# Optimization experiments

Measured on AMD Instinct MI355X. Metric: run time of the kernel, lower is better.

Reference implementation:

```python
import jax, jax.numpy as jnp
import numpy as np

B, C, H, W = 16, 3, 224, 224
P = 16
DIM = 256
NL = 8
DS = 16          # d_state (mamba default)
DCONV = 4
NCLS = 1000
DI = 2 * DIM     # expand * dim
DTR = -(-DIM // 16)  # dt_rank = ceil(dim/16)
NPATCH = (H // P) * (W // P)
SEQ = NPATCH + 1


def _ln(x, g, b, eps=1e-5):
    mu = x.mean(-1, keepdims=True)
    var = ((x - mu) ** 2).mean(-1, keepdims=True)
    return (x - mu) * jax.lax.rsqrt(var + eps) * g + b


def setup_inputs() -> dict:
    key = jax.random.key(0)
    ks = jax.random.split(key, 12)
    pd = C * P * P
    s = 0.02
    return dict(
        img=jax.random.normal(ks[0], (B, C, H, W), jnp.float32),
        pe_ln1_g=jnp.ones((pd,), jnp.float32), pe_ln1_b=jnp.zeros((pd,), jnp.float32),
        pe_w=jax.random.normal(ks[1], (pd, DIM), jnp.float32) * s,
        pe_b=jnp.zeros((DIM,), jnp.float32),
        pe_ln2_g=jnp.ones((DIM,), jnp.float32), pe_ln2_b=jnp.zeros((DIM,), jnp.float32),
        pos_emb=jax.random.normal(ks[2], (1, SEQ, DIM), jnp.float32) * s,
        cls_tok=jax.random.normal(ks[3], (1, 1, DIM), jnp.float32) * s,
        ln_w=jnp.ones((NL, DIM), jnp.float32), ln_b=jnp.zeros((NL, DIM), jnp.float32),
        in_w=jax.random.normal(ks[4], (NL, DIM, 2 * DI), jnp.float32) * s,
        conv_w=jax.random.normal(ks[5], (NL, DI, DCONV), jnp.float32) * s,
        conv_b=jnp.zeros((NL, DI), jnp.float32),
        xproj_w=jax.random.normal(ks[6], (NL, DI, DTR + 2 * DS), jnp.float32) * s,
        dtproj_w=jax.random.normal(ks[7], (NL, DTR, DI), jnp.float32) * s,
        dtproj_b=jax.random.uniform(ks[8], (NL, DI), jnp.float32, -4.0, -2.0),
        A_log=jnp.log(jnp.broadcast_to(jnp.arange(1, DS + 1, dtype=jnp.float32), (NL, DI, DS))) + jnp.zeros((NL, DI, DS), jnp.float32),
        Dp=jnp.ones((NL, DI), jnp.float32),
        out_w=jax.random.normal(ks[9], (NL, DI, DIM), jnp.float32) * s,
        normf_w=jnp.ones((DIM,), jnp.float32), normf_b=jnp.zeros((DIM,), jnp.float32),
        head_w=jax.random.normal(ks[10], (DIM, NCLS), jnp.float32) * s,
        head_b=jnp.zeros((NCLS,), jnp.float32),
    )


def _mamba(x, in_w, conv_w, conv_b, xproj_w, dtproj_w, dtproj_b, A_log, Dp, out_w):
    b, L, _ = x.shape
    xz = x @ in_w                       # (b, L, 2*DI)
    xm, z = jnp.split(xz, 2, axis=-1)
    # causal depthwise conv1d (torch pads both sides then slices -> left-pad d_conv-1)
    xc = jnp.pad(xm.transpose(0, 2, 1), ((0, 0), (0, 0), (DCONV - 1, 0)))
    xc = jax.lax.conv_general_dilated(
        xc, conv_w[:, None, :], (1,), 'VALID',
        dimension_numbers=('NCH', 'OIH', 'NCH'), feature_group_count=DI)
    u = jax.nn.silu(xc + conv_b[None, :, None]).transpose(0, 2, 1)  # (b, L, DI)
    dbc = u @ xproj_w                   # (b, L, DTR+2*DS)
    dt, Bm, Cm = jnp.split(dbc, [DTR, DTR + DS], axis=-1)
    dt = jax.nn.softplus(dt @ dtproj_w + dtproj_b)  # (b, L, DI)
    A = -jnp.exp(A_log)                 # (DI, DS)

    def step(h, inp):
        dt_t, B_t, C_t, u_t = inp       # (b,DI), (b,DS), (b,DS), (b,DI)
        dA = jnp.exp(dt_t[:, :, None] * A)                 # (b, DI, DS)
        h = dA * h + (dt_t * u_t)[:, :, None] * B_t[:, None, :]
        y = jnp.einsum('bdn,bn->bd', h, C_t)
        return h, y

    h0 = jnp.zeros((b, DI, DS), x.dtype)
    xs = (dt.transpose(1, 0, 2), Bm.transpose(1, 0, 2),
          Cm.transpose(1, 0, 2), u.transpose(1, 0, 2))
    _, ys = jax.lax.scan(step, h0, xs)
    y = ys.transpose(1, 0, 2) + u * Dp  # (b, L, DI)
    y = y * jax.nn.silu(z)
    return y @ out_w                    # (b, L, DIM)


def reference(img, pe_ln1_g, pe_ln1_b, pe_w, pe_b, pe_ln2_g, pe_ln2_b, pos_emb,
              cls_tok, ln_w, ln_b, in_w, conv_w, conv_b, xproj_w, dtproj_w,
              dtproj_b, A_log, Dp, out_w, normf_w, normf_b, head_w, head_b):
    b = img.shape[0]
    h, w = H // P, W // P
    # 'b c (h p1) (w p2) -> b (h w) (p1 p2 c)'
    x = img.reshape(b, C, h, P, w, P).transpose(0, 2, 4, 3, 5, 1).reshape(b, h * w, P * P * C)
    x = _ln(x, pe_ln1_g, pe_ln1_b)
    x = x @ pe_w + pe_b
    x = _ln(x, pe_ln2_g, pe_ln2_b)
    x = jnp.concatenate([jnp.broadcast_to(cls_tok, (b, 1, DIM)), x], axis=1)
    x = x + pos_emb[:, :x.shape[1]]
    residual = None
    for i in range(NL):
        residual = x if residual is None else x + residual
        xn = _ln(residual, ln_w[i], ln_b[i])
        x = _mamba(xn, in_w[i], conv_w[i], conv_b[i], xproj_w[i],
                   dtproj_w[i], dtproj_b[i], A_log[i], Dp[i], out_w[i])
    residual = x + residual
    x = _ln(residual, normf_w, normf_b)
    x = x[:, 0]                          # pool == 'cls'
    return x @ head_w + head_b
```

## Files before the change

### kernel.cpp

```cpp
#include <hip/hip_runtime.h>
#include <math.h>

#define NB   16
#define SEQL 197
#define TB   (NB*SEQL)
#define DIMM 256
#define DI   512
#define DS   16
#define NL   8

typedef __bf16 bf16x8 __attribute__((ext_vector_type(8)));
typedef __bf16 bf16x4 __attribute__((ext_vector_type(4)));
typedef float floatx4 __attribute__((ext_vector_type(4)));

__device__ __forceinline__ void block_reduce_2(float& s1, float& s2, float* red, int tid){
  #pragma unroll
  for (int off = 32; off > 0; off >>= 1){
    s1 += __shfl_down(s1, off, 64);
    s2 += __shfl_down(s2, off, 64);
  }
  __syncthreads();
  if ((tid & 63) == 0){ red[(tid>>6)*2] = s1; red[(tid>>6)*2+1] = s2; }
  __syncthreads();
  s1 = red[0] + red[2] + red[4] + red[6];
  s2 = red[1] + red[3] + red[5] + red[7];
}

__global__ __launch_bounds__(256) void transpose_bf16(
    const float* __restrict__ in, __bf16* __restrict__ out, int K, int N)
{
  __shared__ float t[32][33];
  const float* src = in  + (size_t)blockIdx.z*K*N;
  __bf16*      dst = out + (size_t)blockIdx.z*K*N;
  int n0 = blockIdx.x*32, k0 = blockIdx.y*32;
  int tx = threadIdx.x & 31, ty = threadIdx.x >> 5;
  #pragma unroll
  for (int j = 0; j < 4; j++)
    t[ty + j*8][tx] = src[(size_t)(k0 + ty + j*8)*N + n0 + tx];
  __syncthreads();
  #pragma unroll
  for (int j = 0; j < 4; j++)
    dst[(size_t)(n0 + ty + j*8)*K + k0 + tx] = (__bf16)t[tx][ty + j*8];
}

__global__ __launch_bounds__(256) void transpose_bf16_pad(
    const float* __restrict__ in, __bf16* __restrict__ out, int K, int Nin, int Npad)
{
  __shared__ float t[32][33];
  const float* src = in  + (size_t)blockIdx.z*K*Nin;
  __bf16*      dst = out + (size_t)blockIdx.z*Npad*K;
  int n0 = blockIdx.x*32, k0 = blockIdx.y*32;
  int tx = threadIdx.x & 31, ty = threadIdx.x >> 5;
  #pragma unroll
  for (int j = 0; j < 4; j++){
    int n = n0 + tx;
    t[ty + j*8][tx] = (n < Nin) ? src[(size_t)(k0 + ty + j*8)*Nin + n] : 0.f;
  }
  __syncthreads();
  #pragma unroll
  for (int j = 0; j < 4; j++)
    dst[(size_t)(n0 + ty + j*8)*K + k0 + tx] = (__bf16)t[tx][ty + j*8];
}

template<int BM, int BN>
__global__ __launch_bounds__(256) void gemm_bf16(
    const __bf16* __restrict__ A, const __bf16* __restrict__ Wt,
    const float* __restrict__ bias, float* __restrict__ C, int M, int N, int K)
{
  constexpr int BK  = 32;
  constexpr int LDA = BK + 8;
  constexpr int TMW = BM/32;
  constexpr int TNW = BN/32;
  __shared__ __bf16 As[BM][LDA];
  __shared__ __bf16 Bs[BN][LDA];

  int tid  = threadIdx.x;
  int lane = tid & 63, w = tid >> 6;
  int wm = w >> 1, wn = w & 1;
  int l15 = lane & 15, quad = lane >> 4;
  int bm = blockIdx.y * BM, bn = blockIdx.x * BN;

  floatx4 acc[TMW][TNW] = {};

  for (int k0 = 0; k0 < K; k0 += BK){
    #pragma unroll
    for (int i = 0; i < BM/64; i++){
      int c = tid + i*256;
      int row = c >> 2, kc = c & 3;
      int m = bm + row;
      uint4 v = make_uint4(0,0,0,0);
      if (m < M) v = ((const uint4*)(A + (size_t)m*K + k0))[kc];
      *(uint4*)&As[row][kc*8] = v;
    }
    #pragma unroll
    for (int i = 0; i < BN/64; i++){
      int c = tid + i*256;
      int row = c >> 2, kc = c & 3;
      int n = bn + row;
      uint4 v = ((const uint4*)(Wt + (size_t)n*K + k0))[kc];
      *(uint4*)&Bs[row][kc*8] = v;
    }
    __syncthreads();
    bf16x8 af[TMW], bf[TNW];
    #pragma unroll
    for (int mi = 0; mi < TMW; mi++)
      af[mi] = *(const bf16x8*)&As[wm*(BM/2) + mi*16 + l15][quad*8];
    #pragma unroll
    for (int ni = 0; ni < TNW; ni++)
      bf[ni] = *(const bf16x8*)&Bs[wn*(BN/2) + ni*16 + l15][quad*8];
    #pragma unroll
    for (int mi = 0; mi < TMW; mi++)
      #pragma unroll
      for (int ni = 0; ni < TNW; ni++)
        acc[mi][ni] = __builtin_amdgcn_mfma_f32_16x16x32_bf16(af[mi], bf[ni], acc[mi][ni], 0, 0, 0);
    __syncthreads();
  }
  #pragma unroll
  for (int mi = 0; mi < TMW; mi++){
    #pragma unroll
    for (int ni = 0; ni < TNW; ni++){
      int col = bn + wn*(BN/2) + ni*16 + l15;
      float bv = bias ? bias[col] : 0.f;
      #pragma unroll
      for (int r = 0; r < 4; r++){
        int row = bm + wm*(BM/2) + mi*16 + quad*4 + r;
        if (row < M) C[(size_t)row*N + col] = acc[mi][ni][r] + bv;
      }
    }
  }
}

__global__ __launch_bounds__(256) void patch_ln1(
    const float* __restrict__ img, const float* __restrict__ g1, const float* __restrict__ b1,
    __bf16* __restrict__ xp_bf)
{
  __shared__ float red[8];
  int blk = blockIdx.x;
  int b = blk / 196, p = blk % 196;
  int hh = p / 14, ww = p % 14;
  int tid = threadIdx.x;

  float v[3]; float s = 0.f, s2 = 0.f;
  #pragma unroll
  for (int i = 0; i < 3; i++){
    int e  = tid + i*256;
    int c  = e % 3;
    int p2 = (e/3) % 16;
    int p1 = e / 48;
    float val = img[((b*3 + c)*224 + hh*16 + p1)*224 + ww*16 + p2];
    v[i] = val; s += val; s2 += val*val;
  }
  block_reduce_2(s, s2, red, tid);
  float mu = s * (1.f/768.f);
  float var = s2 * (1.f/768.f) - mu*mu;
  float rr = rsqrtf(var + 1e-5f);
  #pragma unroll
  for (int i = 0; i < 3; i++){
    int e = tid + i*256;
    xp_bf[(size_t)blk*768 + e] = (__bf16)((v[i] - mu) * rr * g1[e] + b1[e]);
  }
}

__global__ __launch_bounds__(256) void ln2_pos(
    const float* __restrict__ pemb, const float* __restrict__ g2, const float* __restrict__ b2,
    const float* __restrict__ pos, float* __restrict__ x)
{
  __shared__ float red[8];
  int blk = blockIdx.x;
  int b = blk / 196, p = blk % 196;
  int tid = threadIdx.x;
  float v = pemb[(size_t)blk*256 + tid];
  float s = v, s2 = v*v;
  block_reduce_2(s, s2, red, tid);
  float mu = s * (1.f/256.f);
  float var = s2 * (1.f/256.f) - mu*mu;
  float rr = rsqrtf(var + 1e-5f);
  float o = (v - mu) * rr * g2[tid] + b2[tid] + pos[(1+p)*256 + tid];
  x[((size_t)(b*SEQL + 1 + p))*256 + tid] = o;
}

__global__ __launch_bounds__(256) void cls_pos(
    const float* __restrict__ cls, const float* __restrict__ pos, float* __restrict__ x)
{
  int b = blockIdx.x, tid = threadIdx.x;
  x[(size_t)b*SEQL*256 + tid] = cls[tid] + pos[tid];
}

__global__ __launch_bounds__(256) void add_ln(
    const float* __restrict__ x, float* __restrict__ resid, __bf16* __restrict__ xn_bf,
    const float* __restrict__ g, const float* __restrict__ bta, int first)
{
  int w = threadIdx.x >> 6, l = threadIdx.x & 63;
  int t = blockIdx.x*4 + w;
  size_t base = (size_t)t*256 + l*4;
  float4 xv = *(const float4*)&x[base];
  if (!first){
    float4 rv = *(const float4*)&resid[base];
    xv.x += rv.x; xv.y += rv.y; xv.z += rv.z; xv.w += rv.w;
  }
  *(float4*)&resid[base] = xv;
  float s  = xv.x + xv.y + xv.z + xv.w;
  float s2 = xv.x*xv.x + xv.y*xv.y + xv.z*xv.z + xv.w*xv.w;
  #pragma unroll
  for (int off = 1; off < 64; off <<= 1){
    s  += __shfl_xor(s,  off, 64);
    s2 += __shfl_xor(s2, off, 64);
  }
  float mu = s * (1.f/256.f);
  float var = s2 * (1.f/256.f) - mu*mu;
  float rr = rsqrtf(var + 1e-5f);
  float4 gv = *(const float4*)&g[l*4];
  float4 bv = *(const float4*)&bta[l*4];
  bf16x4 o;
  o[0] = (__bf16)((xv.x - mu)*rr*gv.x + bv.x);
  o[1] = (__bf16)((xv.y - mu)*rr*gv.y + bv.y);
  o[2] = (__bf16)((xv.z - mu)*rr*gv.z + bv.z);
  o[3] = (__bf16)((xv.w - mu)*rr*gv.w + bv.w);
  *(bf16x4*)&xn_bf[base] = o;
}

__global__ __launch_bounds__(256) void conv_silu(
    const float* __restrict__ xz, const float* __restrict__ cw, const float* __restrict__ cb,
    float* __restrict__ u, __bf16* __restrict__ u_bf)
{
  int gid = blockIdx.x*256 + threadIdx.x;
  if (gid >= TB*DI) return;
  int d = gid & 511;
  int t = gid >> 9;
  int l = t % SEQL;
  float acc = cb[d];
  if (l >= 3) acc += xz[(size_t)(t-3)*1024 + d] * cw[d*4+0];
  if (l >= 2) acc += xz[(size_t)(t-2)*1024 + d] * cw[d*4+1];
  if (l >= 1) acc += xz[(size_t)(t-1)*1024 + d] * cw[d*4+2];
  acc += xz[(size_t)t*1024 + d] * cw[d*4+3];
  float sg = 1.f / (1.f + __expf(-acc));
  float val = acc * sg;
  u[(size_t)t*512 + d] = val;
  u_bf[(size_t)t*512 + d] = (__bf16)val;
}

#define SCT 32
#define NCH ((SEQL + SCT - 1)/SCT)
__global__ __launch_bounds__(256) void scan_kernel(
    const float* __restrict__ u, const float* __restrict__ dbc,
    const float* __restrict__ xz, const float* __restrict__ A_log, const float* __restrict__ Dp,
    const float* __restrict__ dtw, const float* __restrict__ dtb,
    __bf16* __restrict__ yg_bf)
{
  __shared__ float s_D [16][36];
  __shared__ float s_B [16][36];
  __shared__ float s_C [16][36];
  __shared__ float s_u [16][36];
  __shared__ float s_z [16][36];
  __shared__ float s_dt[16][36];
  __shared__ float s_yp[SCT][16][20];
  __shared__ float s_dp[16];

  int tid = threadIdx.x;
  int n = tid & 15, dl = tid >> 4;
  int b = blockIdx.x >> 5, dg = blockIdx.x & 31;
  int d0 = dg * 16;
  const size_t base = (size_t)b * SEQL;

  float A = -__expf(A_log[(d0+dl)*DS + n]);
  float h = 0.f;
  if (tid < 16) s_dp[tid] = Dp[d0 + tid];
  float wc[16];
  #pragma unroll
  for (int k = 0; k < 16; k++) wc[k] = dtw[k*512 + d0 + n];
  float dtbv = dtb[d0 + n];

  float r_u[2], r_z[2], r_db[6];
  auto load_regs = [&](int c){
    #pragma unroll
    for (int i = 0; i < 2; i++){
      int v = tid + i*256;
      int tg = c*SCT + (v>>4); if (tg > SEQL-1) tg = SEQL-1;
      size_t t = base + tg;
      r_u[i] = u [t*512 + d0 + (v&15)];
      r_z[i] = xz[t*1024 + 512 + d0 + (v&15)];
    }
    #pragma unroll
    for (int s = 0; s < 3; s++)
      #pragma unroll
      for (int i = 0; i < 2; i++){
        int v = tid + i*256;
        int tg = c*SCT + (v>>4); if (tg > SEQL-1) tg = SEQL-1;
        r_db[s*2+i] = dbc[(base + tg)*64 + s*16 + (v&15)];
      }
  };
  auto write_DBC = [&](){
    #pragma unroll
    for (int i = 0; i < 2; i++){
      int v = tid + i*256;
      s_D[v&15][v>>4] = r_db[0+i];
      s_B[v&15][v>>4] = r_db[2+i];
      s_C[v&15][v>>4] = r_db[4+i];
    }
  };
  auto write_UZ = [&](){
    #pragma unroll
    for (int i = 0; i < 2; i++){
      int v = tid + i*256;
      s_u[v&15][v>>4] = r_u[i];
      s_z[v&15][v>>4] = r_z[i];
    }
  };
  auto compute_dt = [&](){
    #pragma unroll
    for (int i = 0; i < 2; i++){
      int tl = (tid >> 4) + i*16;
      float acc = dtbv;
      #pragma unroll
      for (int k = 0; k < 16; k++) acc += s_D[k][tl] * wc[k];
      s_dt[n][tl] = (acc > 20.f) ? acc : log1pf(__expf(acc));
    }
  };

  load_regs(0);
  write_DBC();
  write_UZ();
  __syncthreads();
  compute_dt();
  __syncthreads();

  for (int c = 0; c < NCH; c++){
    if (c + 1 < NCH) load_regs(c+1);

    float4 dt4, u4, B4, C4;
    #pragma unroll
    for (int tl = 0; tl < SCT; tl++){
      if ((tl & 3) == 0){
        dt4 = *(const float4*)&s_dt[dl][tl];
        u4  = *(const float4*)&s_u [dl][tl];
        B4  = *(const float4*)&s_B [n][tl];
        C4  = *(const float4*)&s_C [n][tl];
      }
      float dtv = ((float*)&dt4)[tl&3];
      float uv  = ((float*)&u4 )[tl&3];
      float Bv  = ((float*)&B4 )[tl&3];
      float Cv  = ((float*)&C4 )[tl&3];
      h = __expf(dtv * A) * h + (dtv * uv) * Bv;
      s_yp[tl][dl][n] = h * Cv;
    }
    __syncthreads();

    if (c + 1 < NCH) write_DBC();

    #pragma unroll
    for (int j = 0; j < 2; j++){
      int p = tid + j*256;
      int tl = p >> 4, dr = p & 15;
      float4 a0 = *(const float4*)&s_yp[tl][dr][0];
      float4 a1 = *(const float4*)&s_yp[tl][dr][4];
      float4 a2 = *(const float4*)&s_yp[tl][dr][8];
      float4 a3 = *(const float4*)&s_yp[tl][dr][12];
      float yv = ((a0.x+a0.y)+(a0.z+a0.w)) + ((a1.x+a1.y)+(a1.z+a1.w))
               + ((a2.x+a2.y)+(a2.z+a2.w)) + ((a3.x+a3.y)+(a3.z+a3.w));
      int tg = c*SCT + tl;
      if (tg < SEQL){
        float uv = s_u[dr][tl];
        float zv = s_z[dr][tl];
        float sg = 1.f / (1.f + __expf(-zv));
        yg_bf[(base + tg)*512 + d0 + dr] = (__bf16)((yv + uv*s_dp[dr]) * zv * sg);
      }
    }
    __syncthreads();

    if (c + 1 < NCH){
      write_UZ();
      compute_dt();
      __syncthreads();
    }
  }
}

__global__ __launch_bounds__(256) void final_ln(
    const float* __restrict__ x, const float* __restrict__ resid,
    const float* __restrict__ g, const float* __restrict__ bta, float* __restrict__ xs_g)
{
  __shared__ float red[8];
  int b = blockIdx.x, tid = threadIdx.x;
  size_t idx = (size_t)b*SEQL*256 + tid;
  float r = x[idx] + resid[idx];
  float s = r, s2 = r*r;
  block_reduce_2(s, s2, red, tid);
  float mu = s * (1.f/256.f);
  float var = s2 * (1.f/256.f) - mu*mu;
  float rr = rsqrtf(var + 1e-5f);
  xs_g[b*256 + tid] = (r - mu) * rr * g[tid] + bta[tid];
}

__global__ __launch_bounds__(256) void head_gemm(
    const float* __restrict__ xs_g, const float* __restrict__ head_w,
    const float* __restrict__ head_b, float* __restrict__ out)
{
  __shared__ float xs[16][256];
  int tid = threadIdx.x;
  #pragma unroll
  for (int i = 0; i < 16; i++) ((float*)xs)[tid + i*256] = xs_g[tid + i*256];
  __syncthreads();
  int nl = tid & 31, bq = tid >> 5;
  int nn = blockIdx.x*32 + nl;
  if (nn >= 1000) return;
  float acc0 = 0.f, acc1 = 0.f;
  #pragma unroll 8
  for (int k = 0; k < 256; k++){
    float w = head_w[k*1000 + nn];
    acc0 += xs[bq][k]   * w;
    acc1 += xs[bq+8][k] * w;
  }
  float hb = head_b[nn];
  out[(size_t)bq*1000 + nn]     = acc0 + hb;
  out[(size_t)(bq+8)*1000 + nn] = acc1 + hb;
}

extern "C" void kernel_launch(void* const* d_in, const int* in_sizes, int n_in,
                              void* d_out, int out_size, void* d_ws, size_t ws_size,
                              hipStream_t stream) {
  const float* img   = (const float*)d_in[0];
  const float* ln1g  = (const float*)d_in[1];
  const float* ln1b  = (const float*)d_in[2];
  const float* pe_w  = (const float*)d_in[3];
  const float* pe_b  = (const float*)d_in[4];
  const float* ln2g  = (const float*)d_in[5];
  const float* ln2b  = (const float*)d_in[6];
  const float* pos   = (const float*)d_in[7];
  const float* cls   = (const float*)d_in[8];
  const float* ln_w  = (const float*)d_in[9];
  const float* ln_b  = (const float*)d_in[10];
  const float* in_w  = (const float*)d_in[11];
  const float* conv_w= (const float*)d_in[12];
  const float* conv_b= (const float*)d_in[13];
  const float* xproj = (const float*)d_in[14];
  const float* dtw   = (const float*)d_in[15];
  const float* dtb   = (const float*)d_in[16];
  const float* A_log = (const float*)d_in[17];
  const float* Dp    = (const float*)d_in[18];
  const float* out_w = (const float*)d_in[19];
  const float* nfw   = (const float*)d_in[20];
  const float* nfb   = (const float*)d_in[21];
  const float* head_w= (const float*)d_in[22];
  const float* head_b= (const float*)d_in[23];
  float* out = (float*)d_out;

  float* ws = (float*)d_ws;
  float* x     = ws;  ws += (size_t)TB*DIMM;
  float* resid = ws;  ws += (size_t)TB*DIMM;
  float* xz    = ws;  ws += (size_t)TB*2*DI;
  float* u     = ws;  ws += (size_t)TB*DI;
  float* dbc   = ws;  ws += (size_t)TB*64;
  float* xs_g  = ws;  ws += (size_t)NB*DIMM;
  __bf16* xn_bf = (__bf16*)ws;  ws += (size_t)TB*DIMM/2;
  __bf16* u_bf  = (__bf16*)ws;  ws += (size_t)TB*DI/2;
  __bf16* yg_bf = (__bf16*)ws;  ws += (size_t)TB*DI/2;
  __bf16* wt_in = (__bf16*)ws;  ws += (size_t)NL*1024*256/2;
  __bf16* wt_out= (__bf16*)ws;  ws += (size_t)NL*256*512/2;
  __bf16* wt_pe = (__bf16*)ws;  ws += (size_t)256*768/2;
  __bf16* wt_xp = (__bf16*)ws;  ws += (size_t)NL*64*512/2;
  __bf16* xp_bf = (__bf16*)xz;
  float*  pemb  = u;

  transpose_bf16<<<dim3(1024/32, 256/32, NL), 256, 0, stream>>>(in_w,  wt_in, 256, 1024);
  transpose_bf16<<<dim3( 256/32, 512/32, NL), 256, 0, stream>>>(out_w, wt_out, 512, 256);
  transpose_bf16<<<dim3( 256/32, 768/32,  1), 256, 0, stream>>>(pe_w,  wt_pe, 768, 256);
  transpose_bf16_pad<<<dim3(2, 512/32, NL), 256, 0, stream>>>(xproj, wt_xp, 512, 48, 64);

  patch_ln1<<<NB*196, 256, 0, stream>>>(img, ln1g, ln1b, xp_bf);
  gemm_bf16<64,64><<<dim3(256/64, 3136/64), 256, 0, stream>>>(
      xp_bf, wt_pe, pe_b, pemb, 3136, 256, 768);
  ln2_pos<<<NB*196, 256, 0, stream>>>(pemb, ln2g, ln2b, pos, x);
  cls_pos<<<NB, 256, 0, stream>>>(cls, pos, x);

  for (int i = 0; i < NL; i++){
    add_ln<<<TB/4, 256, 0, stream>>>(x, resid, xn_bf, ln_w + i*DIMM, ln_b + i*DIMM, i == 0 ? 1 : 0);
    gemm_bf16<64,128><<<dim3(1024/128, (TB+63)/64), 256, 0, stream>>>(
        xn_bf, wt_in + (size_t)i*1024*256, nullptr, xz, TB, 1024, 256);
    conv_silu<<<(TB*DI + 255)/256, 256, 0, stream>>>(xz, conv_w + i*DI*4, conv_b + i*DI, u, u_bf);
    gemm_bf16<64,64><<<dim3(1, (TB+63)/64), 256, 0, stream>>>(
        u_bf, wt_xp + (size_t)i*64*512, nullptr, dbc, TB, 64, 512);
    scan_kernel<<<NB*32, 256, 0, stream>>>(
        u, dbc, xz, A_log + i*DI*DS, Dp + i*DI, dtw + i*16*DI, dtb + i*DI, yg_bf);
    gemm_bf16<64,64><<<dim3(DIMM/64, (TB+63)/64), 256, 0, stream>>>(
        yg_bf, wt_out + (size_t)i*256*512, nullptr, x, TB, DIMM, 512);
  }
  final_ln<<<NB, 256, 0, stream>>>(x, resid, nfw, nfb, xs_g);
  head_gemm<<<(1000+31)/32, 256, 0, stream>>>(xs_g, head_w, head_b, out);
}
```

Before: 725.3 us.

## Prefetch GEMM tiles, add split-K for x_proj, vectorize conv, shuffle-reduce scan

The GEMM kernel now uses BK=64 and prefetches the next tile into registers while the current one is computed. It also gains a split-K template parameter, used with 4 splits and atomicAdd for the narrow x_proj GEMM. conv_silu is vectorized to float4, handling four channels per thread, and zeroes the dbc buffer that the split-K GEMM accumulates into. The scan replaces its large shared-memory partial-sum buffer with wavefront shuffle reductions, and several GEMM tile shapes are enlarged. These changes target launch parallelism, memory bandwidth and LDS traffic, at the cost of atomics, which make results nondeterministic, and higher register pressure.

```diff
diff --git a/kernel.cpp b/kernel.cpp
--- a/kernel.cpp
+++ b/kernel.cpp
@@ -62,15 +62,17 @@
     dst[(size_t)(n0 + ty + j*8)*K + k0 + tx] = (__bf16)t[tx][ty + j*8];
 }
 
-template<int BM, int BN>
+template<int BM, int BN, int KS>
 __global__ __launch_bounds__(256) void gemm_bf16(
     const __bf16* __restrict__ A, const __bf16* __restrict__ Wt,
     const float* __restrict__ bias, float* __restrict__ C, int M, int N, int K)
 {
-  constexpr int BK  = 32;
+  constexpr int BK  = 64;
   constexpr int LDA = BK + 8;
   constexpr int TMW = BM/32;
   constexpr int TNW = BN/32;
+  constexpr int NRA = BM/32;
+  constexpr int NRB = BN/32;
   __shared__ __bf16 As[BM][LDA];
   __shared__ __bf16 Bs[BN][LDA];
 
@@ -78,41 +80,59 @@
   int lane = tid & 63, w = tid >> 6;
   int wm = w >> 1, wn = w & 1;
   int l15 = lane & 15, quad = lane >> 4;
-  int bm = blockIdx.y * BM, bn = blockIdx.x * BN;
+  int nt = blockIdx.x / KS, ks = blockIdx.x % KS;
+  int bm = blockIdx.y * BM, bn = nt * BN;
+  int kbeg = ks * (K / KS), kend = kbeg + (K / KS);
 
   floatx4 acc[TMW][TNW] = {};
-
-  for (int k0 = 0; k0 < K; k0 += BK){
-    #pragma unroll
-    for (int i = 0; i < BM/64; i++){
-      int c = tid + i*256;
-      int row = c >> 2, kc = c & 3;
+  uint4 ra[NRA], rb[NRB];
+
+  auto load_g = [&](int k0){
+    #pragma unroll
+    for (int i = 0; i < NRA; i++){
+      int c = tid + i*256; int row = c >> 3, kc = c & 7;
       int m = bm + row;
-      uint4 v = make_uint4(0,0,0,0);
-      if (m < M) v = ((const uint4*)(A + (size_t)m*K + k0))[kc];
-      *(uint4*)&As[row][kc*8] = v;
-    }
-    #pragma unroll
-    for (int i = 0; i < BN/64; i++){
-      int c = tid + i*256;
-      int row = c >> 2, kc = c & 3;
-      int n = bn + row;
-      uint4 v = ((const uint4*)(Wt + (size_t)n*K + k0))[kc];
-      *(uint4*)&Bs[row][kc*8] = v;
-    }
+      ra[i] = (m < M) ? ((const uint4*)(A + (size_t)m*K + k0))[kc] : make_uint4(0,0,0,0);
+    }
+    #pragma unroll
+    for (int i = 0; i < NRB; i++){
+      int c = tid + i*256; int row = c >> 3, kc = c & 7;
+      rb[i] = ((const uint4*)(Wt + (size_t)(bn+row)*K + k0))[kc];
+    }
+  };
+  auto write_lds = [&](){
+    #pragma unroll
+    for (int i = 0; i < NRA; i++){
+      int c = tid + i*256; int row = c >> 3, kc = c & 7;
+      *(uint4*)&As[row][kc*8] = ra[i];
+    }
+    #pragma unroll
+    for (int i = 0; i < NRB; i++){
+      int c = tid + i*256; int row = c >> 3, kc = c & 7;
+      *(uint4*)&Bs[row][kc*8] = rb[i];
+    }
+  };
+
+  load_g(kbeg);
+  for (int k0 = kbeg; k0 < kend; k0 += BK){
+    write_lds();
     __syncthreads();
-    bf16x8 af[TMW], bf[TNW];
-    #pragma unroll
-    for (int mi = 0; mi < TMW; mi++)
-      af[mi] = *(const bf16x8*)&As[wm*(BM/2) + mi*16 + l15][quad*8];
-    #pragma unroll
-    for (int ni = 0; ni < TNW; ni++)
-      bf[ni] = *(const bf16x8*)&Bs[wn*(BN/2) + ni*16 + l15][quad*8];
-    #pragma unroll
-    for (int mi = 0; mi < TMW; mi++)
+    if (k0 + BK < kend) load_g(k0 + BK);
+    #pragma unroll
+    for (int kc2 = 0; kc2 < BK/32; kc2++){
+      bf16x8 af[TMW], bf[TNW];
+      #pragma unroll
+      for (int mi = 0; mi < TMW; mi++)
+        af[mi] = *(const bf16x8*)&As[wm*(BM/2) + mi*16 + l15][kc2*32 + quad*8];
       #pragma unroll
       for (int ni = 0; ni < TNW; ni++)
-        acc[mi][ni] = __builtin_amdgcn_mfma_f32_16x16x32_bf16(af[mi], bf[ni], acc[mi][ni], 0, 0, 0);
+        bf[ni] = *(const bf16x8*)&Bs[wn*(BN/2) + ni*16 + l15][kc2*32 + quad*8];
+      #pragma unroll
+      for (int mi = 0; mi < TMW; mi++)
+        #pragma unroll
+        for (int ni = 0; ni < TNW; ni++)
+          acc[mi][ni] = __builtin_amdgcn_mfma_f32_16x16x32_bf16(af[mi], bf[ni], acc[mi][ni], 0, 0, 0);
+    }
     __syncthreads();
   }
   #pragma unroll
@@ -120,11 +140,14 @@
     #pragma unroll
     for (int ni = 0; ni < TNW; ni++){
       int col = bn + wn*(BN/2) + ni*16 + l15;
-      float bv = bias ? bias[col] : 0.f;
+      float bv = (KS == 1 && bias) ? bias[col] : 0.f;
       #pragma unroll
       for (int r = 0; r < 4; r++){
         int row = bm + wm*(BM/2) + mi*16 + quad*4 + r;
-        if (row < M) C[(size_t)row*N + col] = acc[mi][ni][r] + bv;
+        if (row < M){
+          if (KS == 1) C[(size_t)row*N + col] = acc[mi][ni][r] + bv;
+          else         atomicAdd(&C[(size_t)row*N + col], acc[mi][ni][r]);
+        }
       }
     }
   }
@@ -221,22 +244,35 @@
 
 __global__ __launch_bounds__(256) void conv_silu(
     const float* __restrict__ xz, const float* __restrict__ cw, const float* __restrict__ cb,
-    float* __restrict__ u, __bf16* __restrict__ u_bf)
+    float* __restrict__ u, __bf16* __restrict__ u_bf, float* __restrict__ dbc)
 {
   int gid = blockIdx.x*256 + threadIdx.x;
-  if (gid >= TB*DI) return;
-  int d = gid & 511;
-  int t = gid >> 9;
+  int dq = gid & 127;
+  int t = gid >> 7;
+  int d = dq*4;
   int l = t % SEQL;
-  float acc = cb[d];
-  if (l >= 3) acc += xz[(size_t)(t-3)*1024 + d] * cw[d*4+0];
-  if (l >= 2) acc += xz[(size_t)(t-2)*1024 + d] * cw[d*4+1];
-  if (l >= 1) acc += xz[(size_t)(t-1)*1024 + d] * cw[d*4+2];
-  acc += xz[(size_t)t*1024 + d] * cw[d*4+3];
-  float sg = 1.f / (1.f + __expf(-acc));
-  float val = acc * sg;
-  u[(size_t)t*512 + d] = val;
-  u_bf[(size_t)t*512 + d] = (__bf16)val;
+  const float4 z4 = make_float4(0.f,0.f,0.f,0.f);
+  float4 x0 = *(const float4*)&xz[(size_t)t*1024 + d];
+  float4 x1 = (l>=1) ? *(const float4*)&xz[(size_t)(t-1)*1024 + d] : z4;
+  float4 x2 = (l>=2) ? *(const float4*)&xz[(size_t)(t-2)*1024 + d] : z4;
+  float4 x3 = (l>=3) ? *(const float4*)&xz[(size_t)(t-3)*1024 + d] : z4;
+  float4 w0 = *(const float4*)&cw[(d+0)*4];
+  float4 w1 = *(const float4*)&cw[(d+1)*4];
+  float4 w2 = *(const float4*)&cw[(d+2)*4];
+  float4 w3 = *(const float4*)&cw[(d+3)*4];
+  float4 r = *(const float4*)&cb[d];
+  r.x += x3.x*w0.x + x2.x*w0.y + x1.x*w0.z + x0.x*w0.w;
+  r.y += x3.y*w1.x + x2.y*w1.y + x1.y*w1.z + x0.y*w1.w;
+  r.z += x3.z*w2.x + x2.z*w2.y + x1.z*w2.z + x0.z*w2.w;
+  r.w += x3.w*w3.x + x2.w*w3.y + x1.w*w3.z + x0.w*w3.w;
+  r.x *= 1.f/(1.f + __expf(-r.x));
+  r.y *= 1.f/(1.f + __expf(-r.y));
+  r.z *= 1.f/(1.f + __expf(-r.z));
+  r.w *= 1.f/(1.f + __expf(-r.w));
+  *(float4*)&u[(size_t)t*512 + d] = r;
+  bf16x4 o; o[0]=(__bf16)r.x; o[1]=(__bf16)r.y; o[2]=(__bf16)r.z; o[3]=(__bf16)r.w;
+  *(bf16x4*)&u_bf[(size_t)t*512 + d] = o;
+  if (d < 64) *(float4*)&dbc[(size_t)t*64 + d] = z4;
 }
 
 #define SCT 32
@@ -253,7 +289,7 @@
   __shared__ float s_u [16][36];
   __shared__ float s_z [16][36];
   __shared__ float s_dt[16][36];
-  __shared__ float s_yp[SCT][16][20];
+  __shared__ float s_y [16][33];
   __shared__ float s_dp[16];
 
   int tid = threadIdx.x;
@@ -327,6 +363,7 @@
   for (int c = 0; c < NCH; c++){
     if (c + 1 < NCH) load_regs(c+1);
 
+    float yreg[SCT];
     float4 dt4, u4, B4, C4;
     #pragma unroll
     for (int tl = 0; tl < SCT; tl++){
@@ -341,24 +378,27 @@
       float Bv  = ((float*)&B4 )[tl&3];
       float Cv  = ((float*)&C4 )[tl&3];
       h = __expf(dtv * A) * h + (dtv * uv) * Bv;
-      s_yp[tl][dl][n] = h * Cv;
+      yreg[tl] = h * Cv;
+    }
+    #pragma unroll
+    for (int tl = 0; tl < SCT; tl++){
+      float y = yreg[tl];
+      y += __shfl_xor(y, 1, 64);
+      y += __shfl_xor(y, 2, 64);
+      y += __shfl_xor(y, 4, 64);
+      y += __shfl_xor(y, 8, 64);
+      if (n == (tl & 15)) s_y[dl][tl] = y;
     }
     __syncthreads();
 
     if (c + 1 < NCH) write_DBC();
-
-    #pragma unroll
-    for (int j = 0; j < 2; j++){
-      int p = tid + j*256;
-      int tl = p >> 4, dr = p & 15;
-      float4 a0 = *(const float4*)&s_yp[tl][dr][0];
-      float4 a1 = *(const float4*)&s_yp[tl][dr][4];
-      float4 a2 = *(const float4*)&s_yp[tl][dr][8];
-      float4 a3 = *(const float4*)&s_yp[tl][dr][12];
-      float yv = ((a0.x+a0.y)+(a0.z+a0.w)) + ((a1.x+a1.y)+(a1.z+a1.w))
-               + ((a2.x+a2.y)+(a2.z+a2.w)) + ((a3.x+a3.y)+(a3.z+a3.w));
+    #pragma unroll
+    for (int i = 0; i < 2; i++){
+      int v = tid + i*256;
+      int tl = v >> 4, dr = v & 15;
       int tg = c*SCT + tl;
       if (tg < SEQL){
+        float yv = s_y[dr][tl];
         float uv = s_u[dr][tl];
         float zv = s_z[dr][tl];
         float sg = 1.f / (1.f + __expf(-zv));
@@ -467,21 +507,22 @@
   transpose_bf16_pad<<<dim3(2, 512/32, NL), 256, 0, stream>>>(xproj, wt_xp, 512, 48, 64);
 
   patch_ln1<<<NB*196, 256, 0, stream>>>(img, ln1g, ln1b, xp_bf);
-  gemm_bf16<64,64><<<dim3(256/64, 3136/64), 256, 0, stream>>>(
+  gemm_bf16<64,128,1><<<dim3(2, 3136/64), 256, 0, stream>>>(
       xp_bf, wt_pe, pe_b, pemb, 3136, 256, 768);
   ln2_pos<<<NB*196, 256, 0, stream>>>(pemb, ln2g, ln2b, pos, x);
   cls_pos<<<NB, 256, 0, stream>>>(cls, pos, x);
 
   for (int i = 0; i < NL; i++){
     add_ln<<<TB/4, 256, 0, stream>>>(x, resid, xn_bf, ln_w + i*DIMM, ln_b + i*DIMM, i == 0 ? 1 : 0);
-    gemm_bf16<64,128><<<dim3(1024/128, (TB+63)/64), 256, 0, stream>>>(
+    gemm_bf16<128,128,1><<<dim3(1024/128, (TB+127)/128), 256, 0, stream>>>(
         xn_bf, wt_in + (size_t)i*1024*256, nullptr, xz, TB, 1024, 256);
-    conv_silu<<<(TB*DI + 255)/256, 256, 0, stream>>>(xz, conv_w + i*DI*4, conv_b + i*DI, u, u_bf);
-    gemm_bf16<64,64><<<dim3(1, (TB+63)/64), 256, 0, stream>>>(
+    conv_silu<<<TB*128/256, 256, 0, stream>>>(
+        xz, conv_w + i*DI*4, conv_b + i*DI, u, u_bf, dbc);
+    gemm_bf16<64,64,4><<<dim3(4, (TB+63)/64), 256, 0, stream>>>(
         u_bf, wt_xp + (size_t)i*64*512, nullptr, dbc, TB, 64, 512);
     scan_kernel<<<NB*32, 256, 0, stream>>>(
         u, dbc, xz, A_log + i*DI*DS, Dp + i*DI, dtw + i*16*DI, dtb + i*DI, yg_bf);
-    gemm_bf16<64,64><<<dim3(DIMM/64, (TB+63)/64), 256, 0, stream>>>(
+    gemm_bf16<64,128,1><<<dim3(2, (TB+63)/64), 256, 0, stream>>>(
         yg_bf, wt_out + (size_t)i*256*512, nullptr, x, TB, DIMM, 512);
   }
   final_ln<<<NB, 256, 0, stream>>>(x, resid, nfw, nfb, xs_g);
```

Result: slower. 1.029 ms (+41.9%).
